# Performance work log

Hardware: AMD Instinct MI355X
Metric: run time of the kernel (lower is better)

## Reference

```python
import jax, jax.numpy as jnp
import numpy as np

MARGIN = 0.3
BIG = 1e5  # same constant the torch code uses to mask out same-id entries for the min


def setup_inputs() -> dict:
    key = jax.random.key(0)
    k1, k2, k3 = jax.random.split(key, 3)
    B, D, N_LUT, N_ID = 4096, 1024, 5000, 1024
    feat = jax.random.normal(k1, (B, D), dtype=jnp.float32)
    lut = jax.random.normal(k2, (N_LUT, D), dtype=jnp.float32)
    id = jax.random.randint(k3, (B,), 0, N_ID, dtype=jnp.int64)
    return {"feat": feat, "lut": lut, "id": id}


def reference(feat, lut, id):
    # feat_oim = lut[id]  (gather rows of the OIM lookup table)
    feat_oim = lut[id]  # (B, D)

    # Pairwise euclidean distance dist[i,j] = sqrt(||feat_i - feat_oim_j||^2 + 1e-12)
    # via the dot-product trick (avoids materializing the (B,B,D) diff tensor).
    sq_a = jnp.sum(feat * feat, axis=1)          # (B,)
    sq_b = jnp.sum(feat_oim * feat_oim, axis=1)  # (B,)
    sq = sq_a[:, None] + sq_b[None, :] - 2.0 * (feat @ feat_oim.T)  # (B, B)
    dist = jnp.sqrt(jnp.maximum(sq, 0.0) + 1e-12)

    # Masks (mode='id'):
    same_id = id[:, None] == id[None, :]               # (B, B) bool
    eye = jnp.eye(feat.shape[0], dtype=bool)
    positive_mask = same_id & ~eye

    # Batch-hard mining (n_dis=0):
    max_positive = jnp.max(dist * positive_mask.astype(dist.dtype), axis=1)   # hardest positive
    min_negative = jnp.min(dist + BIG * same_id.astype(dist.dtype), axis=1)   # hardest negative
    z = max_positive - min_negative

    # float margin path: hinge
    b_loss = jnp.maximum(z + MARGIN, 0.0)  # (B,)
    return b_loss
```

## Files before the change

### kernel.cpp

```cpp
#include <hip/hip_runtime.h>
#include <hip/hip_bf16.h>

#define B_N    4096
#define D_K    1024
#define N_C    1024
#define MARGIN 0.3f
#define BIGM   1e5f

typedef __attribute__((ext_vector_type(8))) short short8;
typedef __attribute__((ext_vector_type(4))) float f32x4;

__device__ inline ushort f2bf(float f) {
    unsigned u = __float_as_uint(f);
    unsigned r = (u + 0x7fffu + ((u >> 16) & 1u)) >> 16;
    return (ushort)r;
}

__device__ inline void async16(const ushort* g, ushort* l) {
    __builtin_amdgcn_global_load_lds(
        (const __attribute__((address_space(1))) void*)g,
        (__attribute__((address_space(3))) void*)l,
        16, 0, 0);
}

__global__ void init_k(int* __restrict__ maxb, int* __restrict__ minb,
                       int* __restrict__ cnt) {
    int i = blockIdx.x * 256 + threadIdx.x;
    maxb[i] = 0;
    minb[i] = 0x7F800000;
    if (i < N_C) cnt[i] = 0;
}

__global__ void prep_all(const float* __restrict__ feat,
                         const float* __restrict__ lut,
                         const int* __restrict__ id,
                         ushort* __restrict__ featB, ushort* __restrict__ lutB,
                         float* __restrict__ sq_a, float* __restrict__ sq_b,
                         int* __restrict__ cnt) {
    int b = blockIdx.x;
    int t = threadIdx.x;
    const float* src; ushort* dst; float* sq;
    if (b < B_N) {
        src = feat + (size_t)b * D_K;
        dst = featB + (size_t)b * D_K;
        sq  = sq_a + b;
        if (t == 0) atomicAdd(cnt + id[b], 1);
    } else {
        int c = b - B_N;
        src = lut + (size_t)c * D_K;
        dst = lutB + (size_t)c * D_K;
        sq  = sq_b + c;
    }
    float4 v = ((const float4*)src)[t];
    float ss = v.x * v.x + v.y * v.y + v.z * v.z + v.w * v.w;
    ushort4 bb;
    bb.x = f2bf(v.x); bb.y = f2bf(v.y); bb.z = f2bf(v.z); bb.w = f2bf(v.w);
    ((ushort4*)dst)[t] = bb;

    int lane = t & 63, w = t >> 6;
    #pragma unroll
    for (int o = 1; o < 64; o <<= 1) ss += __shfl_xor(ss, o);
    __shared__ float red[4];
    if (lane == 0) red[w] = ss;
    __syncthreads();
    if (t == 0) *sq = red[0] + red[1] + red[2] + red[3];
}

__global__ __launch_bounds__(512, 2)
void dist_kernel(const ushort* __restrict__ A, const ushort* __restrict__ Bm,
                 const float* __restrict__ sqa, const float* __restrict__ sqb,
                 const int* __restrict__ ids, const int* __restrict__ cnt,
                 int* __restrict__ maxb, int* __restrict__ minb) {
    __shared__ ushort lds_[3 * 8192];

    const int t = threadIdx.x;
    const int lane = t & 63;
    const int wid = t >> 6;
    const int wr = wid >> 2;
    const int wc = wid & 3;
    const int l15 = lane & 15;
    const int h = lane >> 4;

    const int bid = blockIdx.y * gridDim.x + blockIdx.x;
    const int swz = (bid & 7) * 32 + (bid >> 3);
    const int rb = swz >> 3, cb = swz & 7;

    int p = t * 8;
    int rp = p >> 6;
    int sl = ((p >> 3) & 7) ^ (rp & 7);
    int rr = rp * 2 + (sl >> 2);
    int jj = sl & 3;
    const ushort* gA = A  + (size_t)(rb * 128 + rr) * D_K + jj * 8;
    const ushort* gB = Bm + (size_t)(cb * 128 + rr) * D_K + jj * 8;
    const int lds_wo = wid * 512;

    const int par = (l15 & 1) << 2;
    int offA[4], offB[2];
    {
        int a0 = (wr * 64 + l15) >> 1;
        #pragma unroll
        for (int mf = 0; mf < 4; mf++) {
            int line = a0 + mf * 8;
            offA[mf] = line * 64 + (((par | h) ^ (line & 7)) << 3);
        }
        int b0 = (wc * 32 + l15) >> 1;
        #pragma unroll
        for (int nf = 0; nf < 2; nf++) {
            int line = b0 + nf * 8;
            offB[nf] = line * 64 + (((par | h) ^ (line & 7)) << 3);
        }
    }

    f32x4 acc[4][2] = {};

    async16(gA,      lds_ + lds_wo);
    async16(gB,      lds_ + 4096 + lds_wo);
    async16(gA + 32, lds_ + 8192 + lds_wo);
    async16(gB + 32, lds_ + 8192 + 4096 + lds_wo);

    int s3 = 0, w3 = 2;
    for (int kt = 0; kt < 32; ++kt) {
        const ushort* sA = lds_ + s3 * 8192;
        const ushort* sB = sA + 4096;
        ushort* wbuf = lds_ + w3 * 8192;

        if (kt < 31) asm volatile("s_waitcnt vmcnt(2)" ::: "memory");
        else         asm volatile("s_waitcnt vmcnt(0)" ::: "memory");
        __builtin_amdgcn_sched_barrier(0);
        __builtin_amdgcn_s_barrier();
        __builtin_amdgcn_sched_barrier(0);

        short8 afv[4], bfv[2];
        #pragma unroll
        for (int mf = 0; mf < 4; mf++)
            afv[mf] = *(const short8*)(sA + offA[mf]);
        #pragma unroll
        for (int nf = 0; nf < 2; nf++)
            bfv[nf] = *(const short8*)(sB + offB[nf]);
        if (kt < 30) {
            async16(gA + (kt + 2) * 32, wbuf + lds_wo);
            async16(gB + (kt + 2) * 32, wbuf + 4096 + lds_wo);
        }
        asm volatile("s_waitcnt lgkmcnt(0)" ::: "memory");
        __builtin_amdgcn_sched_barrier(0);
        __builtin_amdgcn_s_setprio(1);
        #pragma unroll
        for (int mf = 0; mf < 4; mf++)
            #pragma unroll
            for (int nf = 0; nf < 2; nf++)
                acc[mf][nf] = __builtin_amdgcn_mfma_f32_16x16x32_bf16(
                    afv[mf], bfv[nf], acc[mf][nf], 0, 0, 0);
        __builtin_amdgcn_s_setprio(0);
        __builtin_amdgcn_sched_barrier(0);
        __builtin_amdgcn_s_barrier();

        s3 = (s3 == 2) ? 0 : s3 + 1;
        w3 = (w3 == 2) ? 0 : w3 + 1;
    }

    int colg[2]; float sb2[2]; int c2[2];
    #pragma unroll
    for (int nf = 0; nf < 2; nf++) {
        int c = cb * 128 + wc * 32 + nf * 16 + l15;
        colg[nf] = c; sb2[nf] = sqb[c]; c2[nf] = cnt[c];
    }
    #pragma unroll
    for (int m = 0; m < 4; m++) {
        #pragma unroll
        for (int r = 0; r < 4; r++) {
            int row = rb * 128 + wr * 64 + m * 16 + h * 4 + r;
            float sa = sqa[row];
            int ida = ids[row];
            float mx = 0.0f, mn = 3.0e38f;
            #pragma unroll
            for (int nf = 0; nf < 2; nf++) {
                float s2 = sa + sb2[nf] - 2.0f * acc[m][nf][r];
                float d = sqrtf(fmaxf(s2, 0.0f) + 1e-12f);
                bool iseq = (colg[nf] == ida);
                float pv = (iseq && c2[nf] >= 2) ? d : 0.0f;
                float nv = (c2[nf] > 0 && !iseq) ? d : 3.0e38f;
                mx = fmaxf(mx, pv);
                mn = fminf(mn, nv);
            }
            #pragma unroll
            for (int o = 1; o < 16; o <<= 1) {
                mx = fmaxf(mx, __shfl_xor(mx, o));
                mn = fminf(mn, __shfl_xor(mn, o));
            }
            if (l15 == 0) {
                atomicMax(maxb + row, __float_as_int(mx));
                atomicMin(minb + row, __float_as_int(mn));
            }
        }
    }
}

__global__ void finalize_k(const int* __restrict__ maxb, const int* __restrict__ minb,
                           float* __restrict__ out) {
    int i = blockIdx.x * blockDim.x + threadIdx.x;
    if (i < B_N) {
        float z = __int_as_float(maxb[i]) - __int_as_float(minb[i]) + MARGIN;
        out[i] = fmaxf(z, 0.0f);
    }
}

extern "C" void kernel_launch(void* const* d_in, const int* in_sizes, int n_in,
                              void* d_out, int out_size, void* d_ws, size_t ws_size,
                              hipStream_t stream) {
    const float* feat = (const float*)d_in[0];
    const float* lut  = (const float*)d_in[1];
    const int*   id   = (const int*)d_in[2];
    float* out = (float*)d_out;

    char* ws = (char*)d_ws;
    ushort* featB = (ushort*)ws;
    ushort* lutB  = (ushort*)(ws + (size_t)B_N * D_K * 2);
    float*  sq_a  = (float*)(ws + (size_t)(B_N + N_C) * D_K * 2);
    float*  sq_b  = sq_a + B_N;
    int*    cnt   = (int*)(sq_b + N_C);
    int*    maxb  = cnt + N_C;
    int*    minb  = maxb + B_N;

    init_k<<<16, 256, 0, stream>>>(maxb, minb, cnt);
    prep_all<<<B_N + N_C, 256, 0, stream>>>(feat, lut, id, featB, lutB,
                                            sq_a, sq_b, cnt);

    dim3 grid(N_C / 128, B_N / 128);
    dist_kernel<<<grid, 512, 0, stream>>>(featB, lutB, sq_a, sq_b, id, cnt,
                                          maxb, minb);

    finalize_k<<<16, 256, 0, stream>>>(maxb, minb, out);
}
```

Before: 41.55 us.

## Deepen GEMM prefetch pipeline to eight LDS stages with tail-specialized waits

Replaces the 3-stage LDS ring in the distance GEMM with an 8-stage ring. Seven K-tiles are prefetched up front, and each iteration issues the load for tile kt+7 after its fragments are read, waiting with vmcnt(12). The tail iterations are peeled so they use decreasing wait counts. This keeps more global loads in flight to hide memory latency, but it grows LDS use to 128KB per block, which may reduce occupancy below the two blocks per CU that the launch bounds request.

```diff
diff --git a/kernel.cpp b/kernel.cpp
--- a/kernel.cpp
+++ b/kernel.cpp
@@ -71,7 +71,7 @@
                  const float* __restrict__ sqa, const float* __restrict__ sqb,
                  const int* __restrict__ ids, const int* __restrict__ cnt,
                  int* __restrict__ maxb, int* __restrict__ minb) {
-    __shared__ ushort lds_[3 * 8192];
+    __shared__ ushort lds_[8 * 8192];
 
     const int t = threadIdx.x;
     const int lane = t & 63;
@@ -113,50 +113,50 @@
 
     f32x4 acc[4][2] = {};
 
-    async16(gA,      lds_ + lds_wo);
-    async16(gB,      lds_ + 4096 + lds_wo);
-    async16(gA + 32, lds_ + 8192 + lds_wo);
-    async16(gB + 32, lds_ + 8192 + 4096 + lds_wo);
-
-    int s3 = 0, w3 = 2;
-    for (int kt = 0; kt < 32; ++kt) {
-        const ushort* sA = lds_ + s3 * 8192;
-        const ushort* sB = sA + 4096;
-        ushort* wbuf = lds_ + w3 * 8192;
-
-        if (kt < 31) asm volatile("s_waitcnt vmcnt(2)" ::: "memory");
-        else         asm volatile("s_waitcnt vmcnt(0)" ::: "memory");
-        __builtin_amdgcn_sched_barrier(0);
-        __builtin_amdgcn_s_barrier();
-        __builtin_amdgcn_sched_barrier(0);
-
-        short8 afv[4], bfv[2];
-        #pragma unroll
-        for (int mf = 0; mf < 4; mf++)
-            afv[mf] = *(const short8*)(sA + offA[mf]);
-        #pragma unroll
-        for (int nf = 0; nf < 2; nf++)
-            bfv[nf] = *(const short8*)(sB + offB[nf]);
-        if (kt < 30) {
-            async16(gA + (kt + 2) * 32, wbuf + lds_wo);
-            async16(gB + (kt + 2) * 32, wbuf + 4096 + lds_wo);
-        }
-        asm volatile("s_waitcnt lgkmcnt(0)" ::: "memory");
-        __builtin_amdgcn_sched_barrier(0);
-        __builtin_amdgcn_s_setprio(1);
-        #pragma unroll
-        for (int mf = 0; mf < 4; mf++)
-            #pragma unroll
-            for (int nf = 0; nf < 2; nf++)
-                acc[mf][nf] = __builtin_amdgcn_mfma_f32_16x16x32_bf16(
-                    afv[mf], bfv[nf], acc[mf][nf], 0, 0, 0);
-        __builtin_amdgcn_s_setprio(0);
-        __builtin_amdgcn_sched_barrier(0);
-        __builtin_amdgcn_s_barrier();
-
-        s3 = (s3 == 2) ? 0 : s3 + 1;
-        w3 = (w3 == 2) ? 0 : w3 + 1;
-    }
+    #pragma unroll
+    for (int kt0 = 0; kt0 < 7; kt0++) {
+        ushort* base = lds_ + kt0 * 8192;
+        async16(gA + kt0 * 32, base + lds_wo);
+        async16(gB + kt0 * 32, base + 4096 + lds_wo);
+    }
+
+#define KITER(KT, VMLIT)                                                    \
+    {                                                                       \
+        const int sb_ = ((KT) & 7) * 8192;                                  \
+        asm volatile("s_waitcnt vmcnt(" VMLIT ")" ::: "memory");            \
+        __builtin_amdgcn_sched_barrier(0);                                  \
+        __builtin_amdgcn_s_barrier();             \
+        __builtin_amdgcn_sched_barrier(0);                                  \
+        short8 afv[4], bfv[2];                                              \
+        _Pragma("unroll") for (int mf = 0; mf < 4; mf++)                    \
+            afv[mf] = *(const short8*)(lds_ + sb_ + offA[mf]);              \
+        _Pragma("unroll") for (int nf = 0; nf < 2; nf++)                    \
+            bfv[nf] = *(const short8*)(lds_ + sb_ + 4096 + offB[nf]);       \
+        asm volatile("s_waitcnt lgkmcnt(0)" ::: "memory");                  \
+        __builtin_amdgcn_sched_barrier(0);                                  \
+        __builtin_amdgcn_s_barrier();              \
+        if ((KT) + 7 < 32) {               \
+            ushort* wb_ = lds_ + (((KT) + 7) & 7) * 8192;                   \
+            async16(gA + ((KT) + 7) * 32, wb_ + lds_wo);                    \
+            async16(gB + ((KT) + 7) * 32, wb_ + 4096 + lds_wo);             \
+        }                                                                   \
+        __builtin_amdgcn_s_setprio(1);                                      \
+        _Pragma("unroll") for (int mf = 0; mf < 4; mf++)                    \
+            _Pragma("unroll") for (int nf = 0; nf < 2; nf++)                \
+                acc[mf][nf] = __builtin_amdgcn_mfma_f32_16x16x32_bf16(      \
+                    afv[mf], bfv[nf], acc[mf][nf], 0, 0, 0);                \
+        __builtin_amdgcn_s_setprio(0);                                      \
+        __builtin_amdgcn_sched_barrier(0);                                  \
+    }
+
+    for (int kt = 0; kt < 26; ++kt) KITER(kt, "12");
+    KITER(26, "10");
+    KITER(27, "8");
+    KITER(28, "6");
+    KITER(29, "4");
+    KITER(30, "2");
+    KITER(31, "0");
+#undef KITER
 
     int colg[2]; float sb2[2]; int c2[2];
     #pragma unroll
```

After: 41.47 us. No clear change (-0.2%).

## Shrink GEMM tiles to 64x64 with double buffering and fold init into prep

Applied to the files above, without the earlier changes.

The distance GEMM moves from 128x128 tiles with 512 threads and triple-buffered LDS to 64x64 tiles with 256 threads, double buffering, and more blocks per CU. This gives 1024 blocks instead of 256, so the CUs are filled better. The cost is less data reuse per tile and more global loads. The init kernel is folded into prep_all, and per-id counts now come from a single block using an LDS histogram instead of global atomics, which removes one launch. The prefetch now happens before the barrier with a depth of one stage, which reduces latency hiding.

```diff
diff --git a/kernel.cpp b/kernel.cpp
--- a/kernel.cpp
+++ b/kernel.cpp
@@ -23,28 +23,39 @@
         16, 0, 0);
 }
 
-__global__ void init_k(int* __restrict__ maxb, int* __restrict__ minb,
-                       int* __restrict__ cnt) {
-    int i = blockIdx.x * 256 + threadIdx.x;
-    maxb[i] = 0;
-    minb[i] = 0x7F800000;
-    if (i < N_C) cnt[i] = 0;
-}
-
 __global__ void prep_all(const float* __restrict__ feat,
                          const float* __restrict__ lut,
                          const int* __restrict__ id,
                          ushort* __restrict__ featB, ushort* __restrict__ lutB,
                          float* __restrict__ sq_a, float* __restrict__ sq_b,
-                         int* __restrict__ cnt) {
+                         int* __restrict__ cnt,
+                         int* __restrict__ maxb, int* __restrict__ minb) {
     int b = blockIdx.x;
     int t = threadIdx.x;
+
+    if (b == B_N + N_C) {
+        __shared__ int hc[N_C];
+        #pragma unroll
+        for (int i = 0; i < 4; i++) hc[t * 4 + i] = 0;
+        __syncthreads();
+        #pragma unroll
+        for (int i = 0; i < 16; i++) atomicAdd(&hc[id[t * 16 + i]], 1);
+        __syncthreads();
+        #pragma unroll
+        for (int i = 0; i < 4; i++) cnt[t * 4 + i] = hc[t * 4 + i];
+        return;
+    }
+
+    if (b < 16) {
+        int i = b * 256 + t;
+        maxb[i] = 0;
+        minb[i] = 0x7F800000;
+    }
     const float* src; ushort* dst; float* sq;
     if (b < B_N) {
         src = feat + (size_t)b * D_K;
         dst = featB + (size_t)b * D_K;
         sq  = sq_a + b;
-        if (t == 0) atomicAdd(cnt + id[b], 1);
     } else {
         int c = b - B_N;
         src = lut + (size_t)c * D_K;
@@ -66,40 +77,40 @@
     if (t == 0) *sq = red[0] + red[1] + red[2] + red[3];
 }
 
-__global__ __launch_bounds__(512, 2)
+__global__ __launch_bounds__(256, 4)
 void dist_kernel(const ushort* __restrict__ A, const ushort* __restrict__ Bm,
                  const float* __restrict__ sqa, const float* __restrict__ sqb,
                  const int* __restrict__ ids, const int* __restrict__ cnt,
                  int* __restrict__ maxb, int* __restrict__ minb) {
-    __shared__ ushort lds_[3 * 8192];
+    __shared__ ushort lds_[2 * 4096];
 
     const int t = threadIdx.x;
     const int lane = t & 63;
     const int wid = t >> 6;
-    const int wr = wid >> 2;
-    const int wc = wid & 3;
+    const int wr = wid >> 1;
+    const int wc = wid & 1;
     const int l15 = lane & 15;
     const int h = lane >> 4;
+    const int wo = wid * 512;
 
     const int bid = blockIdx.y * gridDim.x + blockIdx.x;
-    const int swz = (bid & 7) * 32 + (bid >> 3);
-    const int rb = swz >> 3, cb = swz & 7;
+    const int swz = (bid & 7) * 128 + (bid >> 3);
+    const int rb = swz >> 4, cb = swz & 15;
 
     int p = t * 8;
     int rp = p >> 6;
     int sl = ((p >> 3) & 7) ^ (rp & 7);
     int rr = rp * 2 + (sl >> 2);
     int jj = sl & 3;
-    const ushort* gA = A  + (size_t)(rb * 128 + rr) * D_K + jj * 8;
-    const ushort* gB = Bm + (size_t)(cb * 128 + rr) * D_K + jj * 8;
-    const int lds_wo = wid * 512;
+    const ushort* gA = A  + (size_t)(rb * 64 + rr) * D_K + jj * 8;
+    const ushort* gB = Bm + (size_t)(cb * 64 + rr) * D_K + jj * 8;
 
     const int par = (l15 & 1) << 2;
-    int offA[4], offB[2];
+    int offA[2], offB[2];
     {
-        int a0 = (wr * 64 + l15) >> 1;
-        #pragma unroll
-        for (int mf = 0; mf < 4; mf++) {
+        int a0 = (wr * 32 + l15) >> 1;
+        #pragma unroll
+        for (int mf = 0; mf < 2; mf++) {
             int line = a0 + mf * 8;
             offA[mf] = line * 64 + (((par | h) ^ (line & 7)) << 3);
         }
@@ -111,41 +122,40 @@
         }
     }
 
-    f32x4 acc[4][2] = {};
-
-    async16(gA,      lds_ + lds_wo);
-    async16(gB,      lds_ + 4096 + lds_wo);
-    async16(gA + 32, lds_ + 8192 + lds_wo);
-    async16(gB + 32, lds_ + 8192 + 4096 + lds_wo);
-
-    int s3 = 0, w3 = 2;
+    f32x4 acc[2][2] = {};
+
+    async16(gA, lds_ + wo);
+    async16(gB, lds_ + 2048 + wo);
+
     for (int kt = 0; kt < 32; ++kt) {
-        const ushort* sA = lds_ + s3 * 8192;
-        const ushort* sB = sA + 4096;
-        ushort* wbuf = lds_ + w3 * 8192;
-
-        if (kt < 31) asm volatile("s_waitcnt vmcnt(2)" ::: "memory");
-        else         asm volatile("s_waitcnt vmcnt(0)" ::: "memory");
+        const int s = kt & 1;
+        const ushort* sA = lds_ + s * 4096;
+        const ushort* sB = sA + 2048;
+
+        if (kt < 31) {
+            ushort* wb = lds_ + (s ^ 1) * 4096;
+            async16(gA + (kt + 1) * 32, wb + wo);
+            async16(gB + (kt + 1) * 32, wb + 2048 + wo);
+            asm volatile("s_waitcnt vmcnt(2)" ::: "memory");
+        } else {
+            asm volatile("s_waitcnt vmcnt(0)" ::: "memory");
+        }
         __builtin_amdgcn_sched_barrier(0);
         __builtin_amdgcn_s_barrier();
         __builtin_amdgcn_sched_barrier(0);
 
-        short8 afv[4], bfv[2];
-        #pragma unroll
-        for (int mf = 0; mf < 4; mf++)
+        short8 afv[2], bfv[2];
+        #pragma unroll
+        for (int mf = 0; mf < 2; mf++)
             afv[mf] = *(const short8*)(sA + offA[mf]);
         #pragma unroll
         for (int nf = 0; nf < 2; nf++)
             bfv[nf] = *(const short8*)(sB + offB[nf]);
-        if (kt < 30) {
-            async16(gA + (kt + 2) * 32, wbuf + lds_wo);
-            async16(gB + (kt + 2) * 32, wbuf + 4096 + lds_wo);
-        }
         asm volatile("s_waitcnt lgkmcnt(0)" ::: "memory");
         __builtin_amdgcn_sched_barrier(0);
         __builtin_amdgcn_s_setprio(1);
         #pragma unroll
-        for (int mf = 0; mf < 4; mf++)
+        for (int mf = 0; mf < 2; mf++)
             #pragma unroll
             for (int nf = 0; nf < 2; nf++)
                 acc[mf][nf] = __builtin_amdgcn_mfma_f32_16x16x32_bf16(
@@ -153,22 +163,19 @@
         __builtin_amdgcn_s_setprio(0);
         __builtin_amdgcn_sched_barrier(0);
         __builtin_amdgcn_s_barrier();
-
-        s3 = (s3 == 2) ? 0 : s3 + 1;
-        w3 = (w3 == 2) ? 0 : w3 + 1;
     }
 
     int colg[2]; float sb2[2]; int c2[2];
     #pragma unroll
     for (int nf = 0; nf < 2; nf++) {
-        int c = cb * 128 + wc * 32 + nf * 16 + l15;
+        int c = cb * 64 + wc * 32 + nf * 16 + l15;
         colg[nf] = c; sb2[nf] = sqb[c]; c2[nf] = cnt[c];
     }
     #pragma unroll
-    for (int m = 0; m < 4; m++) {
+    for (int m = 0; m < 2; m++) {
         #pragma unroll
         for (int r = 0; r < 4; r++) {
-            int row = rb * 128 + wr * 64 + m * 16 + h * 4 + r;
+            int row = rb * 64 + wr * 32 + m * 16 + h * 4 + r;
             float sa = sqa[row];
             int ida = ids[row];
             float mx = 0.0f, mn = 3.0e38f;
@@ -221,12 +228,11 @@
     int*    maxb  = cnt + N_C;
     int*    minb  = maxb + B_N;
 
-    init_k<<<16, 256, 0, stream>>>(maxb, minb, cnt);
-    prep_all<<<B_N + N_C, 256, 0, stream>>>(feat, lut, id, featB, lutB,
-                                            sq_a, sq_b, cnt);
-
-    dim3 grid(N_C / 128, B_N / 128);
-    dist_kernel<<<grid, 512, 0, stream>>>(featB, lutB, sq_a, sq_b, id, cnt,
+    prep_all<<<B_N + N_C + 1, 256, 0, stream>>>(feat, lut, id, featB, lutB,
+                                                sq_a, sq_b, cnt, maxb, minb);
+
+    dim3 grid(N_C / 64, B_N / 64);
+    dist_kernel<<<grid, 256, 0, stream>>>(featB, lutB, sq_a, sq_b, id, cnt,
                                           maxb, minb);
 
     finalize_k<<<16, 256, 0, stream>>>(maxb, minb, out);
```

New measurement: 39.46 us. 1.05x faster.
